# Kernel tuning notes

Hardware: AMD Instinct MI355X
Metric: run time of the kernel (lower is better)

Reference implementation:

```python
import jax, jax.numpy as jnp
import numpy as np

B, L = 4, 40960
C = 512
DMLP = 2048
TEMP = 1e-5
EPS = 1e-5
FACTOR = 2  # Smartpool factor at layer 4


def setup_inputs() -> dict:
    key = jax.random.key(0)
    ks = jax.random.split(key, 8)

    def w(k, shape, fan_in):
        return jax.random.normal(k, shape, jnp.float32) / np.float32(np.sqrt(fan_in))

    inp = {
        "x": jax.random.normal(ks[0], (B, 1, L), jnp.float32),
        "conv0_w": w(ks[1], (C, 1, 10), 10),   "conv0_b": jnp.zeros(C, jnp.float32),
        "conv1_w": w(ks[2], (C, C, 8), C * 8), "conv1_b": jnp.zeros(C, jnp.float32),
        "conv2_w": w(ks[3], (C, C, 4), C * 4), "conv2_b": jnp.zeros(C, jnp.float32),
        "conv3_w": w(ks[4], (C, C, 4), C * 4), "conv3_b": jnp.zeros(C, jnp.float32),
        "mlp_w1": w(ks[5], (C, DMLP), C),       "mlp_b1": jnp.zeros(DMLP, jnp.float32),
        "mlp_w2": w(ks[6], (DMLP, DMLP), DMLP), "mlp_b2": jnp.zeros(DMLP, jnp.float32),
        "mlp_w3": w(ks[7], (DMLP, 1), DMLP),    "mlp_b3": jnp.zeros(1, jnp.float32),
    }
    for i in range(5):  # ChannelNorm affine params (init: ones/zeros)
        inp[f"n{i}_w"] = jnp.ones(C, jnp.float32)
        inp[f"n{i}_b"] = jnp.zeros(C, jnp.float32)
    return inp


def _conv(x, w, b, stride, pad):
    # Conv1d with padding_mode='reflect': reflect-pad then VALID conv. x: [B,C,T]
    x = jnp.pad(x, ((0, 0), (0, 0), (pad, pad)), mode="reflect")
    y = jax.lax.conv_general_dilated(x, w, (stride,), "VALID",
                                     dimension_numbers=("NCH", "OIH", "NCH"))
    return y + b[None, :, None]


def _cnorm(x, g, b):
    # ChannelNorm: normalize over channel dim with unbiased variance (torch.var default)
    m = jnp.mean(x, axis=1, keepdims=True)
    v = jnp.var(x, axis=1, keepdims=True, ddof=1)
    return (x - m) * jax.lax.rsqrt(v + EPS) * g[None, :, None] + b[None, :, None]


def _forward(x, conv0_w, conv0_b, conv1_w, conv1_b, conv2_w, conv2_b, conv3_w, conv3_b,
             n0_w, n0_b, n1_w, n1_b, n2_w, n2_b, n3_w, n3_b, n4_w, n4_b,
             mlp_w1, mlp_b1, mlp_w2, mlp_b2, mlp_w3, mlp_b3):
    h = jax.nn.relu(_cnorm(_conv(x, conv0_w, conv0_b, 5, 3), n0_w, n0_b))
    h = jax.nn.relu(_cnorm(_conv(h, conv1_w, conv1_b, 4, 2), n1_w, n1_b))
    h = jax.nn.relu(_cnorm(_conv(h, conv2_w, conv2_b, 2, 1), n2_w, n2_b))
    h = jax.nn.relu(_cnorm(_conv(h, conv3_w, conv3_b, 2, 1), n3_w, n3_b))

    f = jnp.transpose(h, (0, 2, 1))  # [B,T,C]
    T = f.shape[1]

    # importance MLP (dropout inactive in eval), exact GELU, sigmoid head
    z = jax.nn.gelu(f @ mlp_w1 + mlp_b1, approximate=False)
    z = jax.nn.gelu(z @ mlp_w2 + mlp_b2, approximate=False)
    imp = jax.nn.sigmoid((z @ mlp_w3 + mlp_b3)[..., 0]) + TEMP          # [B,T]
    imp = imp / jnp.sum(imp, axis=1, keepdims=True) * (T / FACTOR)      # sums to T/factor

    # warp: cumsum -> ramp contributions -> 2x2 [[-1,1],[1,-1]] conv = double diff
    Tn = T // FACTOR  # == round(importance_cs[0,-1])
    cs = jnp.cumsum(imp, axis=1)                                        # [B,T]
    p = jnp.maximum(cs[:, :, None] - jnp.arange(Tn, dtype=cs.dtype)[None, None, :], 0.0)  # [B,T,Tn]
    pc = jnp.pad(p, ((0, 0), (0, 0), (0, 1)))
    d = pc[:, :, :-1] - pc[:, :, 1:]                                    # diff along new-time axis
    wmat = d - jnp.pad(d, ((0, 0), (1, 0), (0, 0)))[:, :-1, :]          # diff along old-time axis, [B,T,Tn]
    pooled = jnp.einsum("btn,btc->bnc", wmat, f)                        # interp_weights @ X

    out = jnp.transpose(pooled, (0, 2, 1))                              # [B,C,Tn]
    return jax.nn.relu(_cnorm(out, n4_w, n4_b))


def reference(x, conv0_w, conv0_b, conv1_w, conv1_b, conv2_w, conv2_b, conv3_w, conv3_b,
              n0_w, n0_b, n1_w, n1_b, n2_w, n2_b, n3_w, n3_b, n4_w, n4_b,
              mlp_w1, mlp_b1, mlp_w2, mlp_b2, mlp_w3, mlp_b3):
    return _forward(x, conv0_w, conv0_b, conv1_w, conv1_b, conv2_w, conv2_b, conv3_w, conv3_b,
                    n0_w, n0_b, n1_w, n1_b, n2_w, n2_b, n3_w, n3_b, n4_w, n4_b,
                    mlp_w1, mlp_b1, mlp_w2, mlp_b2, mlp_w3, mlp_b3)
```

## Files before the change

kernel.cpp:

```cpp
#include <hip/hip_runtime.h>
#include <hip/hip_bf16.h>
#include <math.h>

#define NB 4
#define LIN 40960
#define NC 512
#define T0 8192
#define T1 2048
#define T2 1024
#define T3 512
#define TN 256
#define DM 2048
#define EPSF 1e-5f
#define TEMPF 1e-5f

typedef __attribute__((ext_vector_type(8))) short bf16x8;
typedef __attribute__((ext_vector_type(4))) float f32x4;

__device__ __forceinline__ int refl(int t, int T) {
  if (t < 0) t = -t;
  if (t >= T) t = 2 * T - 2 - t;
  return t;
}

__device__ __forceinline__ void gld16(void* lds, const void* g) {
  __builtin_amdgcn_global_load_lds((const __attribute__((address_space(1))) unsigned int*)g,
                                   (__attribute__((address_space(3))) unsigned int*)lds, 16, 0, 0);
}

__device__ __forceinline__ void blk_sum2_512(float& a, float& b, float* scratch) {
#pragma unroll
  for (int off = 32; off > 0; off >>= 1) {
    a += __shfl_down(a, off, 64);
    b += __shfl_down(b, off, 64);
  }
  int lane = threadIdx.x & 63, wid = threadIdx.x >> 6;
  __syncthreads();
  if (lane == 0) { scratch[wid] = a; scratch[8 + wid] = b; }
  __syncthreads();
  float sa = 0.f, sb = 0.f;
#pragma unroll
  for (int i = 0; i < 8; i++) { sa += scratch[i]; sb += scratch[8 + i]; }
  a = sa; b = sb;
}

__device__ __forceinline__ void add_bf8(const __hip_bfloat16* p, float* v) {
  union { uint4 u; __hip_bfloat16 h[8]; } pk;
  pk.u = *(const uint4*)p;
#pragma unroll
  for (int j = 0; j < 8; j++) v[j] += __bfloat162float(pk.h[j]);
}

template <int KT>
__device__ __forceinline__ void prep_conv_body(const float* __restrict__ w, __hip_bfloat16* __restrict__ wt,
                                               int co, float* l) {
  const float* wb = w + (size_t)co * 512 * KT;
  for (int i = threadIdx.x; i < 512 * KT; i += 512) l[i] = wb[i];
  __syncthreads();
  __hip_bfloat16* wo = wt + (size_t)co * 512 * KT;
  for (int i = threadIdx.x; i < 512 * KT; i += 512) {
    int kk = i >> 9, ci = i & 511;
    wo[i] = __float2bfloat16(l[ci * KT + kk]);
  }
}

template <int KD, int ND>
__device__ __forceinline__ void prep_mlp_body(const float* __restrict__ w, __hip_bfloat16* __restrict__ wt,
                                              int bidx, float* sbuf) {
  float(*tile)[33] = (float(*)[33])sbuf;
  int bx = bidx % (ND / 32);
  int by = bidx / (ND / 32);
  int tx = threadIdx.x & 31, ty = threadIdx.x >> 5;
#pragma unroll
  for (int i = 0; i < 32; i += 16)
    tile[ty + i][tx] = w[(size_t)(by * 32 + ty + i) * ND + bx * 32 + tx];
  __syncthreads();
#pragma unroll
  for (int i = 0; i < 32; i += 16)
    wt[(size_t)(bx * 32 + ty + i) * KD + by * 32 + tx] = __float2bfloat16(tile[tx][ty + i]);
}

__device__ __forceinline__ void conv0_body(const float* __restrict__ x, const float* __restrict__ w,
                                           const float* __restrict__ bias, const float* __restrict__ gw,
                                           const float* __restrict__ gb, __hip_bfloat16* __restrict__ out,
                                           int blk, float* smem) {
  float* xv = smem;
  float* tb = smem + 64;
  float* stats = smem + 4672;
  int b = blk / (T0 / 8);
  int t0 = (blk % (T0 / 8)) * 8;
  int tid = threadIdx.x;
  if (tid < 45) xv[tid] = x[(size_t)b * LIN + refl(t0 * 5 - 3 + tid, LIN)];
  __syncthreads();
  float wk[10];
#pragma unroll
  for (int k = 0; k < 10; k++) wk[k] = w[tid * 10 + k];
  float bs = bias[tid];
  float acc[8];
#pragma unroll
  for (int tt = 0; tt < 8; tt++) {
    float a = bs;
#pragma unroll
    for (int k = 0; k < 10; k++) a += xv[tt * 5 + k] * wk[k];
    acc[tt] = a;
    tb[tid * 9 + tt] = a;
  }
  __syncthreads();
  int wave = tid >> 6, lane = tid & 63;
  float s = 0.f, q = 0.f;
#pragma unroll
  for (int j = 0; j < 8; j++) {
    float v = tb[(lane * 8 + j) * 9 + wave];
    s += v; q += v * v;
  }
#pragma unroll
  for (int off = 32; off > 0; off >>= 1) {
    s += __shfl_xor(s, off, 64);
    q += __shfl_xor(q, off, 64);
  }
  if (lane == 0) {
    float mean = s * (1.f / NC);
    float var = fmaxf((q - s * s * (1.f / NC)) * (1.f / (NC - 1)), 0.f);
    stats[wave] = mean;
    stats[8 + wave] = rsqrtf(var + EPSF);
  }
  __syncthreads();
  float gwv = gw[tid], gbv = gb[tid];
#pragma unroll
  for (int tt = 0; tt < 8; tt++) {
    float y = (acc[tt] - stats[tt]) * stats[8 + tt] * gwv + gbv;
    out[((size_t)(b * T0 + t0 + tt)) * NC + tid] = __float2bfloat16(fmaxf(y, 0.f));
  }
}

__global__ __launch_bounds__(512) void k_init(const float* x, const float* c0w, const float* c0b,
                                              const float* n0w, const float* n0b, __hip_bfloat16* h0b,
                                              const float* c1w, const float* c2w, const float* c3w,
                                              const float* mw1, const float* mw2,
                                              __hip_bfloat16* wt1, __hip_bfloat16* wt2,
                                              __hip_bfloat16* wt3, __hip_bfloat16* wm1t,
                                              __hip_bfloat16* wm2t) {
  __shared__ float smem[4688];
  int b = blockIdx.x;
  if (b < 4096) conv0_body(x, c0w, c0b, n0w, n0b, h0b, b, smem);
  else if (b < 4608) prep_conv_body<8>(c1w, wt1, b - 4096, smem);
  else if (b < 5120) prep_conv_body<4>(c2w, wt2, b - 4608, smem);
  else if (b < 5632) prep_conv_body<4>(c3w, wt3, b - 5120, smem);
  else if (b < 6656) prep_mlp_body<512, 2048>(mw1, wm1t, b - 5632, smem);
  else prep_mlp_body<2048, 2048>(mw2, wm2t, b - 6656, smem);
}

template <int MODE, int TIN_, int TOUT_, int SS, int PP, int KK, int NN, int SPLITK, int MM>
__global__ __launch_bounds__(256) void k_gemmB(const __hip_bfloat16* __restrict__ A,
                                               const __hip_bfloat16* __restrict__ Bt,
                                               __hip_bfloat16* __restrict__ Cp) {
  __shared__ __align__(16) __hip_bfloat16 sA[2][128 * 32];
  __shared__ __align__(16) __hip_bfloat16 sB[2][2][128 * 32];
  const int tid = threadIdx.x;
  const int lane = tid & 63;
  const int wave = tid >> 6;
  const int wm = wave >> 1, wn = wave & 1;
  constexpr int nt = NN / 128;
  constexpr int PS = (MM / 1024) * nt;
  constexpr int KBT = KK / 32;
  const int blk = blockIdx.x;
  const int xs = blk & 7, sl = blk >> 3;
  const int sk = sl / PS, rem = sl % PS;
  const int row0 = ((rem / nt) * 8 + xs) * 128;
  const int col0 = (rem % nt) * 128;
  const int kb0 = (sk * KBT) / SPLITK, kb1 = ((sk + 1) * KBT) / SPLITK;
  const int cq = lane >> 4, cl = lane & 15;

  const char* aP[2];
  const char* bP[2];

  auto stageA = [&](int kb, int buf) {
    bool recalc = (kb == kb0) || (MODE == 1 && (kb & 15) == 0);
    if (recalc) {
#pragma unroll
      for (int rr = 0; rr < 2; rr++) {
        int c = rr * 256 + tid;
        int m = c >> 2, kc = c & 3;
        int kcs = kc ^ (m & 3);
        size_t ga;
        if (MODE == 0) {
          ga = (size_t)(row0 + m) * KK + kb * 32 + kcs * 8;
        } else {
          int r = row0 + m;
          int bb = r / TOUT_;
          int t = r - bb * TOUT_;
          int k = (kb * 32) >> 9;
          int ci = ((kb * 32) & 511) + kcs * 8;
          int gt = refl(t * SS - PP + k, TIN_);
          ga = (((size_t)(bb * TIN_ + gt)) << 9) + ci;
        }
        aP[rr] = (const char*)(A + ga);
      }
    }
#pragma unroll
    for (int rr = 0; rr < 2; rr++) {
      gld16((char*)&sA[buf][0] + (rr * 256 + tid) * 16, aP[rr]);
      aP[rr] += 64;
    }
  };

  auto stageB = [&](int buf, bool doSub1) {
#pragma unroll
    for (int rr = 0; rr < 2; rr++) {
      gld16((char*)&sB[buf][0][0] + (rr * 256 + tid) * 16, bP[rr]);
      if (doSub1) gld16((char*)&sB[buf][1][0] + (rr * 256 + tid) * 16, bP[rr] + 64);
      bP[rr] += 128;
    }
  };

#pragma unroll
  for (int rr = 0; rr < 2; rr++) {
    int c = rr * 256 + tid;
    int n = c >> 2, kc = c & 3;
    int kcs = kc ^ (n & 3);
    bP[rr] = (const char*)(Bt + (size_t)(col0 + n) * KK + kb0 * 32 + kcs * 8);
  }

  f32x4 acc[4][4];
  const f32x4 zz = {0.f, 0.f, 0.f, 0.f};
#pragma unroll
  for (int mi = 0; mi < 4; mi++)
#pragma unroll
    for (int ni = 0; ni < 4; ni++) acc[mi][ni] = zz;

  stageA(kb0, 0);
  stageB(0, kb0 + 1 < kb1);

  const int p = cq ^ (cl & 3);
  for (int kb = kb0; kb < kb1; kb++) {
    const int jj = kb - kb0;
    __syncthreads();
    if (kb + 1 < kb1) stageA(kb + 1, (jj + 1) & 1);
    if (((jj & 1) == 0) && (kb + 2 < kb1)) stageB(((jj >> 1) + 1) & 1, kb + 3 < kb1);
    const short* bA = (const short*)&sA[jj & 1][0];
    const short* bB = (const short*)&sB[(jj >> 1) & 1][jj & 1][0];
    bf16x8 af[4], bfr[4];
#pragma unroll
    for (int mi = 0; mi < 4; mi++)
      af[mi] = *(const bf16x8*)(bA + (wm * 64 + mi * 16 + cl) * 32 + p * 8);
#pragma unroll
    for (int ni = 0; ni < 4; ni++)
      bfr[ni] = *(const bf16x8*)(bB + (wn * 64 + ni * 16 + cl) * 32 + p * 8);
#pragma unroll
    for (int mi = 0; mi < 4; mi++)
#pragma unroll
      for (int ni = 0; ni < 4; ni++)
        acc[mi][ni] = __builtin_amdgcn_mfma_f32_16x16x32_bf16(af[mi], bfr[ni], acc[mi][ni], 0, 0, 0);
  }

#pragma unroll
  for (int mi = 0; mi < 4; mi++)
#pragma unroll
    for (int ni = 0; ni < 4; ni++)
#pragma unroll
      for (int r2 = 0; r2 < 4; r2++) {
        int row = row0 + wm * 64 + mi * 16 + cq * 4 + r2;
        int col = col0 + wn * 64 + ni * 16 + cl;
        Cp[(size_t)sk * MM * NN + (size_t)row * NN + col] = __float2bfloat16(acc[mi][ni][r2]);
      }
}

template <int MODE, int TIN_, int TOUT_, int SS, int PP, int KK, int NN, int EPI, int SPLITK, int MM>
__global__ __launch_bounds__(256, 4) void k_gemmC(const __hip_bfloat16* __restrict__ A,
                                                  const __hip_bfloat16* __restrict__ Bt,
                                                  const float* __restrict__ bias,
                                                  __hip_bfloat16* __restrict__ Cout) {
  __shared__ __align__(16) __hip_bfloat16 sA[2][64 * 32];
  __shared__ __align__(16) __hip_bfloat16 sB[2][2][128 * 32];
  const int tid = threadIdx.x;
  const int lane = tid & 63;
  const int wave = tid >> 6;
  const int wm = wave >> 1, wn = wave & 1;
  constexpr int nt = NN / 128;
  constexpr int PS = (MM / 512) * nt;
  constexpr int KBT = KK / 32;
  const int blk = blockIdx.x;
  const int xs = blk & 7, sl = blk >> 3;
  const int sk = sl / PS, rem = sl % PS;
  const int row0 = ((rem / nt) * 8 + xs) * 64;
  const int col0 = (rem % nt) * 128;
  const int kb0 = (sk * KBT) / SPLITK, kb1 = ((sk + 1) * KBT) / SPLITK;
  const int cq = lane >> 4, cl = lane & 15;

  const char* aP;
  const char* bP[2];

  auto stageA = [&](int kb, int buf) {
    bool recalc = (kb == kb0) || (MODE == 1 && (kb & 15) == 0);
    if (recalc) {
      int m = tid >> 2, kc = tid & 3;
      int kcs = kc ^ (m & 3);
      size_t ga;
      if (MODE == 0) {
        ga = (size_t)(row0 + m) * KK + kb * 32 + kcs * 8;
      } else {
        int r = row0 + m;
        int bb = r / TOUT_;
        int t = r - bb * TOUT_;
        int k = (kb * 32) >> 9;
        int ci = ((kb * 32) & 511) + kcs * 8;
        int gt = refl(t * SS - PP + k, TIN_);
        ga = (((size_t)(bb * TIN_ + gt)) << 9) + ci;
      }
      aP = (const char*)(A + ga);
    }
    gld16((char*)&sA[buf][0] + tid * 16, aP);
    aP += 64;
  };

  auto stageB = [&](int buf, bool doSub1) {
#pragma unroll
    for (int rr = 0; rr < 2; rr++) {
      gld16((char*)&sB[buf][0][0] + (rr * 256 + tid) * 16, bP[rr]);
      if (doSub1) gld16((char*)&sB[buf][1][0] + (rr * 256 + tid) * 16, bP[rr] + 64);
      bP[rr] += 128;
    }
  };

#pragma unroll
  for (int rr = 0; rr < 2; rr++) {
    int c = rr * 256 + tid;
    int n = c >> 2, kc = c & 3;
    int kcs = kc ^ (n & 3);
    bP[rr] = (const char*)(Bt + (size_t)(col0 + n) * KK + kb0 * 32 + kcs * 8);
  }

  f32x4 acc[2][4];
  const f32x4 zz = {0.f, 0.f, 0.f, 0.f};
#pragma unroll
  for (int mi = 0; mi < 2; mi++)
#pragma unroll
    for (int ni = 0; ni < 4; ni++) acc[mi][ni] = zz;

  stageA(kb0, 0);
  stageB(0, kb0 + 1 < kb1);

  const int p = cq ^ (cl & 3);
  for (int kb = kb0; kb < kb1; kb++) {
    const int jj = kb - kb0;
    __syncthreads();
    if (kb + 1 < kb1) stageA(kb + 1, (jj + 1) & 1);
    if (((jj & 1) == 0) && (kb + 2 < kb1)) stageB(((jj >> 1) + 1) & 1, kb + 3 < kb1);
    const short* bA = (const short*)&sA[jj & 1][0];
    const short* bB = (const short*)&sB[(jj >> 1) & 1][jj & 1][0];
    bf16x8 af[2], bfr[4];
#pragma unroll
    for (int mi = 0; mi < 2; mi++)
      af[mi] = *(const bf16x8*)(bA + (wm * 32 + mi * 16 + cl) * 32 + p * 8);
#pragma unroll
    for (int ni = 0; ni < 4; ni++)
      bfr[ni] = *(const bf16x8*)(bB + (wn * 64 + ni * 16 + cl) * 32 + p * 8);
#pragma unroll
    for (int mi = 0; mi < 2; mi++)
#pragma unroll
      for (int ni = 0; ni < 4; ni++)
        acc[mi][ni] = __builtin_amdgcn_mfma_f32_16x16x32_bf16(af[mi], bfr[ni], acc[mi][ni], 0, 0, 0);
  }

#pragma unroll
  for (int mi = 0; mi < 2; mi++)
#pragma unroll
    for (int ni = 0; ni < 4; ni++)
#pragma unroll
      for (int r2 = 0; r2 < 4; r2++) {
        int row = row0 + wm * 32 + mi * 16 + cq * 4 + r2;
        int col = col0 + wn * 64 + ni * 16 + cl;
        float v = acc[mi][ni][r2];
        if (EPI == 1) {
          v += bias[col];
          v = 0.5f * v * (1.f + erff(v * 0.70710678118654752f));
          Cout[(size_t)row * NN + col] = __float2bfloat16(v);
        } else {
          Cout[(size_t)sk * MM * NN + (size_t)row * NN + col] = __float2bfloat16(v);
        }
      }
}

template <int NS>
__global__ __launch_bounds__(512) void k_cnorm(const __hip_bfloat16* __restrict__ g,
                                               const float* __restrict__ cb,
                                               const float* __restrict__ gw, const float* __restrict__ gb,
                                               __hip_bfloat16* __restrict__ out, size_t stride) {
  int wave = threadIdx.x >> 6, lane = threadIdx.x & 63;
  size_t row = (size_t)blockIdx.x * 8 + wave;
  float v[8];
  {
    float4 c0 = *(const float4*)(cb + lane * 8), c1 = *(const float4*)(cb + lane * 8 + 4);
    v[0] = c0.x; v[1] = c0.y; v[2] = c0.z; v[3] = c0.w;
    v[4] = c1.x; v[5] = c1.y; v[6] = c1.z; v[7] = c1.w;
  }
#pragma unroll
  for (int s = 0; s < NS; s++) add_bf8(g + s * stride + row * NC + lane * 8, v);
  float s = 0.f, q = 0.f;
#pragma unroll
  for (int j = 0; j < 8; j++) { s += v[j]; q += v[j] * v[j]; }
#pragma unroll
  for (int off = 32; off > 0; off >>= 1) {
    s += __shfl_xor(s, off, 64);
    q += __shfl_xor(q, off, 64);
  }
  float mean = s * (1.f / NC);
  float var = fmaxf((q - s * s * (1.f / NC)) * (1.f / (NC - 1)), 0.f);
  float rstd = rsqrtf(var + EPSF);
  float4 w0 = *(const float4*)(gw + lane * 8), w1 = *(const float4*)(gw + lane * 8 + 4);
  float4 b0 = *(const float4*)(gb + lane * 8), b1 = *(const float4*)(gb + lane * 8 + 4);
  float gwv[8] = {w0.x, w0.y, w0.z, w0.w, w1.x, w1.y, w1.z, w1.w};
  float gbv[8] = {b0.x, b0.y, b0.z, b0.w, b1.x, b1.y, b1.z, b1.w};
  union { __hip_bfloat16 h[8]; uint4 u; } pk;
#pragma unroll
  for (int j = 0; j < 8; j++)
    pk.h[j] = __float2bfloat16(fmaxf((v[j] - mean) * rstd * gwv[j] + gbv[j], 0.f));
  *(uint4*)(out + row * NC + lane * 8) = pk.u;
}

template <int NS>
__global__ __launch_bounds__(256) void k_head(const __hip_bfloat16* __restrict__ g,
                                              const float* __restrict__ b2,
                                              const float* __restrict__ w3, const float* __restrict__ b3,
                                              float* __restrict__ imp) {
  __shared__ float red[4];
  int row = blockIdx.x, tid = threadIdx.x;
  int c = tid * 8;
  float v[8];
  {
    float4 x0 = *(const float4*)(b2 + c), x1 = *(const float4*)(b2 + c + 4);
    v[0] = x0.x; v[1] = x0.y; v[2] = x0.z; v[3] = x0.w;
    v[4] = x1.x; v[5] = x1.y; v[6] = x1.z; v[7] = x1.w;
  }
#pragma unroll
  for (int s = 0; s < NS; s++) add_bf8(g + (size_t)s * (2048 * DM) + (size_t)row * DM + c, v);
  float a = 0.f;
  float4 w0 = *(const float4*)(w3 + c), w1 = *(const float4*)(w3 + c + 4);
  float wv[8] = {w0.x, w0.y, w0.z, w0.w, w1.x, w1.y, w1.z, w1.w};
#pragma unroll
  for (int j = 0; j < 8; j++) {
    float z = 0.5f * v[j] * (1.f + erff(v[j] * 0.70710678118654752f));
    a += z * wv[j];
  }
#pragma unroll
  for (int off = 32; off > 0; off >>= 1) a += __shfl_down(a, off, 64);
  int lane = tid & 63, wid = tid >> 6;
  if (lane == 0) red[wid] = a;
  __syncthreads();
  if (tid == 0) {
    float s = red[0] + red[1] + red[2] + red[3] + b3[0];
    imp[row] = 1.f / (1.f + expf(-s)) + TEMPF;
  }
}

__device__ __forceinline__ float dfun(float cv, int n) {
  float d = fmaxf(cv - (float)n, 0.f);
  if (n < TN - 1) d = fminf(d, 1.f);
  return d;
}

__global__ __launch_bounds__(512) void k_poolfinal(const __hip_bfloat16* __restrict__ f,
                                                   const float* __restrict__ imp,
                                                   const float* __restrict__ gw, const float* __restrict__ gb,
                                                   float* __restrict__ out) {
  __shared__ float wt[T3];
  __shared__ float wsum[8];
  __shared__ float red[16];
  int b = blockIdx.x / TN, n = blockIdx.x % TN;
  int tid = threadIdx.x, wave = tid >> 6, lane = tid & 63;
  float own = imp[b * T3 + tid];
  float s = own;
#pragma unroll
  for (int off = 1; off < 64; off <<= 1) {
    float t = __shfl_up(s, off, 64);
    if (lane >= off) s += t;
  }
  if (lane == 63) wsum[wave] = s;
  __syncthreads();
  float prefix = 0.f, total = 0.f;
#pragma unroll
  for (int w = 0; w < 8; w++) {
    float ws_ = wsum[w];
    total += ws_;
    if (w < wave) prefix += ws_;
  }
  float scale = (float)TN / total;
  float incl = (prefix + s) * scale;
  float excl = (prefix + s - own) * scale;
  wt[tid] = dfun(incl, n) - dfun(excl, n);
  __syncthreads();
  float acc = 0.f;
  for (int t = 0; t < T3; t++) {
    float w = wt[t];
    if (w != 0.f) acc += w * __bfloat162float(f[((size_t)b * T3 + t) * NC + tid]);
  }
  float sv = acc, q = acc * acc;
  blk_sum2_512(sv, q, red);
  float mean = sv * (1.f / NC);
  float var = fmaxf((q - sv * sv * (1.f / NC)) * (1.f / (NC - 1)), 0.f);
  float y = (acc - mean) * rsqrtf(var + EPSF) * gw[tid] + gb[tid];
  out[((size_t)b * NC + tid) * TN + n] = fmaxf(y, 0.f);
}

extern "C" void kernel_launch(void* const* d_in, const int* in_sizes, int n_in,
                              void* d_out, int out_size, void* d_ws, size_t ws_size,
                              hipStream_t stream) {
  const float* x   = (const float*)d_in[0];
  const float* c0w = (const float*)d_in[1];  const float* c0b = (const float*)d_in[2];
  const float* c1w = (const float*)d_in[3];  const float* c1b = (const float*)d_in[4];
  const float* c2w = (const float*)d_in[5];  const float* c2b = (const float*)d_in[6];
  const float* c3w = (const float*)d_in[7];  const float* c3b = (const float*)d_in[8];
  const float* mw1 = (const float*)d_in[9];  const float* mb1 = (const float*)d_in[10];
  const float* mw2 = (const float*)d_in[11]; const float* mb2 = (const float*)d_in[12];
  const float* mw3 = (const float*)d_in[13]; const float* mb3 = (const float*)d_in[14];
  const float* n0w = (const float*)d_in[15]; const float* n0b = (const float*)d_in[16];
  const float* n1w = (const float*)d_in[17]; const float* n1b = (const float*)d_in[18];
  const float* n2w = (const float*)d_in[19]; const float* n2b = (const float*)d_in[20];
  const float* n3w = (const float*)d_in[21]; const float* n3b = (const float*)d_in[22];
  const float* n4w = (const float*)d_in[23]; const float* n4b = (const float*)d_in[24];

  char* base = (char*)d_ws;
  __hip_bfloat16* h0b  = (__hip_bfloat16*)(base);
  __hip_bfloat16* h1b  = (__hip_bfloat16*)(base);
  __hip_bfloat16* h2b  = (__hip_bfloat16*)(base + (8u << 20));
  __hip_bfloat16* h3b  = (__hip_bfloat16*)(base + (12u << 20));
  __hip_bfloat16* z1b  = (__hip_bfloat16*)(base + (14u << 20));
  float*          imp  = (float*)(base + (22u << 20));
  __hip_bfloat16* g    = (__hip_bfloat16*)(base + (32u << 20));
  __hip_bfloat16* wm1t = (__hip_bfloat16*)(base + (64u << 20));
  __hip_bfloat16* wt2  = (__hip_bfloat16*)(base + (66u << 20));
  __hip_bfloat16* wt3  = (__hip_bfloat16*)(base + (68u << 20));
  __hip_bfloat16* wt1  = (__hip_bfloat16*)(base + (70u << 20));
  __hip_bfloat16* wm2t = (__hip_bfloat16*)(base + (74u << 20));
  float* outp = (float*)d_out;

  k_init<<<4096 + 6656, 512, 0, stream>>>(x, c0w, c0b, n0w, n0b, h0b,
                                          c1w, c2w, c3w, mw1, mw2, wt1, wt2, wt3, wm1t, wm2t);

  k_gemmB<1, 8192, 2048, 4, 2, 4096, 512, 3, 8192><<<768, 256, 0, stream>>>(h0b, wt1, g);
  k_cnorm<3><<<8192 / 8, 512, 0, stream>>>(g, c1b, n1w, n1b, h1b, (size_t)8192 * 512);
  k_gemmB<1, 2048, 1024, 2, 1, 2048, 512, 6, 4096><<<768, 256, 0, stream>>>(h1b, wt2, g);
  k_cnorm<6><<<4096 / 8, 512, 0, stream>>>(g, c2b, n2w, n2b, h2b, (size_t)4096 * 512);
  k_gemmC<1, 1024, 512, 2, 1, 2048, 512, 0, 6, 2048><<<768, 256, 0, stream>>>(h2b, wt3, c3b, g);
  k_cnorm<6><<<2048 / 8, 512, 0, stream>>>(g, c3b, n3w, n3b, h3b, (size_t)2048 * 512);
  k_gemmC<0, 0, 1, 0, 0, 512, 2048, 1, 1, 2048><<<512, 256, 0, stream>>>(h3b, wm1t, mb1, z1b);
  k_gemmB<0, 0, 1, 0, 0, 2048, 2048, 3, 2048><<<768, 256, 0, stream>>>(z1b, wm2t, g);

  k_head<3><<<NB * T3, 256, 0, stream>>>(g, mb2, mw3, mb3, imp);
  k_poolfinal<<<NB * TN, 512, 0, stream>>>(h3b, imp, n4w, n4b, outp);
}
```

Measured before the change: 315.1 us.

## Switch GEMM kernels to triple-buffered LDS pipeline with explicit vmcnt waits

Both bf16 MFMA GEMM kernels used double buffering of A, with B loaded two k-steps at a time, and a full __syncthreads each step. They now use a three-slot ring for A and B, prefetching two k-steps ahead. Each step waits with a partial s_waitcnt vmcnt so only the oldest stage must have landed, then issues a raw s_barrier. This keeps more global loads in flight and drops the full drain at every barrier, but LDS use goes up and correctness depends on the hand-set vmcnt counts matching the number of loads issued per stage.

```diff
diff --git a/kernel.cpp b/kernel.cpp
--- a/kernel.cpp
+++ b/kernel.cpp
@@ -154,8 +154,8 @@
 __global__ __launch_bounds__(256) void k_gemmB(const __hip_bfloat16* __restrict__ A,
                                                const __hip_bfloat16* __restrict__ Bt,
                                                __hip_bfloat16* __restrict__ Cp) {
-  __shared__ __align__(16) __hip_bfloat16 sA[2][128 * 32];
-  __shared__ __align__(16) __hip_bfloat16 sB[2][2][128 * 32];
+  __shared__ __align__(16) __hip_bfloat16 sA[3][128 * 32];
+  __shared__ __align__(16) __hip_bfloat16 sB[3][128 * 32];
   const int tid = threadIdx.x;
   const int lane = tid & 63;
   const int wave = tid >> 6;
@@ -204,12 +204,11 @@
     }
   };
 
-  auto stageB = [&](int buf, bool doSub1) {
+  auto stageB = [&](int buf) {
 #pragma unroll
     for (int rr = 0; rr < 2; rr++) {
-      gld16((char*)&sB[buf][0][0] + (rr * 256 + tid) * 16, bP[rr]);
-      if (doSub1) gld16((char*)&sB[buf][1][0] + (rr * 256 + tid) * 16, bP[rr] + 64);
-      bP[rr] += 128;
+      gld16((char*)&sB[buf][0] + (rr * 256 + tid) * 16, bP[rr]);
+      bP[rr] += 64;
     }
   };
 
@@ -228,17 +227,20 @@
 #pragma unroll
     for (int ni = 0; ni < 4; ni++) acc[mi][ni] = zz;
 
+  const int NS = kb1 - kb0;
   stageA(kb0, 0);
-  stageB(0, kb0 + 1 < kb1);
+  stageB(0);
+  if (NS > 1) { stageA(kb0 + 1, 1); stageB(1); }
 
   const int p = cq ^ (cl & 3);
-  for (int kb = kb0; kb < kb1; kb++) {
-    const int jj = kb - kb0;
-    __syncthreads();
-    if (kb + 1 < kb1) stageA(kb + 1, (jj + 1) & 1);
-    if (((jj & 1) == 0) && (kb + 2 < kb1)) stageB(((jj >> 1) + 1) & 1, kb + 3 < kb1);
-    const short* bA = (const short*)&sA[jj & 1][0];
-    const short* bB = (const short*)&sB[(jj >> 1) & 1][jj & 1][0];
+  int slot = 0, slot2 = 2;
+  for (int jj = 0; jj < NS; ++jj) {
+    if (jj + 1 < NS) { asm volatile("s_waitcnt vmcnt(4)" ::: "memory"); }
+    else             { asm volatile("s_waitcnt vmcnt(0)" ::: "memory"); }
+    __builtin_amdgcn_s_barrier();
+    if (jj + 2 < NS) { stageA(kb0 + jj + 2, slot2); stageB(slot2); }
+    const short* bA = (const short*)&sA[slot][0];
+    const short* bB = (const short*)&sB[slot][0];
     bf16x8 af[4], bfr[4];
 #pragma unroll
     for (int mi = 0; mi < 4; mi++)
@@ -251,6 +253,8 @@
 #pragma unroll
       for (int ni = 0; ni < 4; ni++)
         acc[mi][ni] = __builtin_amdgcn_mfma_f32_16x16x32_bf16(af[mi], bfr[ni], acc[mi][ni], 0, 0, 0);
+    slot = (slot == 2) ? 0 : slot + 1;
+    slot2 = (slot2 == 2) ? 0 : slot2 + 1;
   }
 
 #pragma unroll
@@ -270,8 +274,8 @@
                                                   const __hip_bfloat16* __restrict__ Bt,
                                                   const float* __restrict__ bias,
                                                   __hip_bfloat16* __restrict__ Cout) {
-  __shared__ __align__(16) __hip_bfloat16 sA[2][64 * 32];
-  __shared__ __align__(16) __hip_bfloat16 sB[2][2][128 * 32];
+  __shared__ __align__(16) __hip_bfloat16 sA[3][64 * 32];
+  __shared__ __align__(16) __hip_bfloat16 sB[3][128 * 32];
   const int tid = threadIdx.x;
   const int lane = tid & 63;
   const int wave = tid >> 6;
@@ -313,12 +317,11 @@
     aP += 64;
   };
 
-  auto stageB = [&](int buf, bool doSub1) {
+  auto stageB = [&](int buf) {
 #pragma unroll
     for (int rr = 0; rr < 2; rr++) {
-      gld16((char*)&sB[buf][0][0] + (rr * 256 + tid) * 16, bP[rr]);
-      if (doSub1) gld16((char*)&sB[buf][1][0] + (rr * 256 + tid) * 16, bP[rr] + 64);
-      bP[rr] += 128;
+      gld16((char*)&sB[buf][0] + (rr * 256 + tid) * 16, bP[rr]);
+      bP[rr] += 64;
     }
   };
 
@@ -337,17 +340,20 @@
 #pragma unroll
     for (int ni = 0; ni < 4; ni++) acc[mi][ni] = zz;
 
+  const int NS = kb1 - kb0;
   stageA(kb0, 0);
-  stageB(0, kb0 + 1 < kb1);
+  stageB(0);
+  if (NS > 1) { stageA(kb0 + 1, 1); stageB(1); }
 
   const int p = cq ^ (cl & 3);
-  for (int kb = kb0; kb < kb1; kb++) {
-    const int jj = kb - kb0;
-    __syncthreads();
-    if (kb + 1 < kb1) stageA(kb + 1, (jj + 1) & 1);
-    if (((jj & 1) == 0) && (kb + 2 < kb1)) stageB(((jj >> 1) + 1) & 1, kb + 3 < kb1);
-    const short* bA = (const short*)&sA[jj & 1][0];
-    const short* bB = (const short*)&sB[(jj >> 1) & 1][jj & 1][0];
+  int slot = 0, slot2 = 2;
+  for (int jj = 0; jj < NS; ++jj) {
+    if (jj + 1 < NS) { asm volatile("s_waitcnt vmcnt(3)" ::: "memory"); }
+    else             { asm volatile("s_waitcnt vmcnt(0)" ::: "memory"); }
+    __builtin_amdgcn_s_barrier();
+    if (jj + 2 < NS) { stageA(kb0 + jj + 2, slot2); stageB(slot2); }
+    const short* bA = (const short*)&sA[slot][0];
+    const short* bB = (const short*)&sB[slot][0];
     bf16x8 af[2], bfr[4];
 #pragma unroll
     for (int mi = 0; mi < 2; mi++)
@@ -360,6 +366,8 @@
 #pragma unroll
       for (int ni = 0; ni < 4; ni++)
         acc[mi][ni] = __builtin_amdgcn_mfma_f32_16x16x32_bf16(af[mi], bfr[ni], acc[mi][ni], 0, 0, 0);
+    slot = (slot == 2) ? 0 : slot + 1;
+    slot2 = (slot2 == 2) ? 0 : slot2 + 1;
   }
 
 #pragma unroll
```

Result: no change. 320.3 us (+1.7%).

## Add 256x256-tile split-K GEMM kernel for conv1 and MLP layer 2

Applied to the files above, without the earlier changes.

Adds a new GEMM kernel using 256x256 output tiles, 512 threads (8 waves), and double-buffered LDS stages that each hold two 32-wide K slices. Global loads for the next stage are interleaved across the four compute sub-steps, and the kernel raises wave priority around the MFMA block. It replaces the 128-tile kernel for conv1 and the second MLP layer, with split-K raised from 3 to 4 and the downstream reductions updated to match. Larger tiles cut redundant global/LDS traffic per FLOP, but the grid shrinks to 256 blocks. The kernel also needs more registers and LDS, which could hurt occupancy.

```diff
diff --git a/kernel.cpp b/kernel.cpp
--- a/kernel.cpp
+++ b/kernel.cpp
@@ -148,6 +148,152 @@
   else if (b < 5632) prep_conv_body<4>(c3w, wt3, b - 5120, smem);
   else if (b < 6656) prep_mlp_body<512, 2048>(mw1, wm1t, b - 5632, smem);
   else prep_mlp_body<2048, 2048>(mw2, wm2t, b - 6656, smem);
+}
+
+template <int MODE, int TIN_, int TOUT_, int SS, int PP, int KK, int NN, int SPLITK, int MM>
+__global__ __launch_bounds__(512, 2) void k_gemmE(const __hip_bfloat16* __restrict__ A,
+                                                  const __hip_bfloat16* __restrict__ Bt,
+                                                  __hip_bfloat16* __restrict__ Cp) {
+  __shared__ __align__(16) __hip_bfloat16 sA[2][2][256 * 32];
+  __shared__ __align__(16) __hip_bfloat16 sB[2][2][256 * 32];
+  const int tid = threadIdx.x;
+  const int lane = tid & 63;
+  const int wave = tid >> 6;
+  const int wm = wave >> 2, wn = wave & 3;
+  constexpr int nt = NN / 256;
+  constexpr int PS = (MM / 2048) * nt;
+  constexpr int KBT = KK / 32;
+  constexpr int NT = KBT / (2 * SPLITK);
+  const int blk = blockIdx.x;
+  const int xs = blk & 7, sl = blk >> 3;
+  const int sk = sl / PS, rem = sl % PS;
+  const int row0 = ((rem / nt) * 8 + xs) * 256;
+  const int col0 = (rem % nt) * 256;
+  const int kb0 = sk * (KBT / SPLITK);
+  const int cq = lane >> 4, cl = lane & 15;
+
+  const char* aP[2];
+  const char* bP[2];
+
+  auto stageA = [&](int kb, int buf, int kk) {
+    bool recalc = (kb == kb0) || (MODE == 1 && (kb & 15) == 0);
+    if (recalc) {
+#pragma unroll
+      for (int rr = 0; rr < 2; rr++) {
+        int c = rr * 512 + tid;
+        int m = c >> 2, kc = c & 3;
+        int kcs = kc ^ (m & 3);
+        size_t ga;
+        if (MODE == 0) {
+          ga = (size_t)(row0 + m) * KK + kb * 32 + kcs * 8;
+        } else {
+          int r = row0 + m;
+          int bb = r / TOUT_;
+          int t = r - bb * TOUT_;
+          int k = (kb * 32) >> 9;
+          int ci = ((kb * 32) & 511) + kcs * 8;
+          int gt = refl(t * SS - PP + k, TIN_);
+          ga = (((size_t)(bb * TIN_ + gt)) << 9) + ci;
+        }
+        aP[rr] = (const char*)(A + ga);
+      }
+    }
+#pragma unroll
+    for (int rr = 0; rr < 2; rr++) {
+      gld16((char*)&sA[buf][kk][0] + (rr * 512 + tid) * 16, aP[rr]);
+      aP[rr] += 64;
+    }
+  };
+
+  auto stageB = [&](int buf, int kk) {
+#pragma unroll
+    for (int rr = 0; rr < 2; rr++) {
+      gld16((char*)&sB[buf][kk][0] + (rr * 512 + tid) * 16, bP[rr]);
+      bP[rr] += 64;
+    }
+  };
+
+#pragma unroll
+  for (int rr = 0; rr < 2; rr++) {
+    int c = rr * 512 + tid;
+    int n = c >> 2, kc = c & 3;
+    int kcs = kc ^ (n & 3);
+    bP[rr] = (const char*)(Bt + (size_t)(col0 + n) * KK + kb0 * 32 + kcs * 8);
+  }
+
+  f32x4 acc[8][4];
+  const f32x4 zz = {0.f, 0.f, 0.f, 0.f};
+#pragma unroll
+  for (int mi = 0; mi < 8; mi++)
+#pragma unroll
+    for (int ni = 0; ni < 4; ni++) acc[mi][ni] = zz;
+
+  stageA(kb0, 0, 0);
+  stageB(0, 0);
+  stageA(kb0 + 1, 0, 1);
+  stageB(0, 1);
+  asm volatile("s_waitcnt vmcnt(0)" ::: "memory");
+  __builtin_amdgcn_s_barrier();
+
+  const int p = cq ^ (cl & 3);
+  for (int t = 0; t < NT; ++t) {
+    const int buf = t & 1;
+    const int kbase = kb0 + 2 * t;
+    const short* bA0 = (const short*)&sA[buf][0][0];
+    const short* bA1 = (const short*)&sA[buf][1][0];
+    const short* bB0 = (const short*)&sB[buf][0][0];
+    const short* bB1 = (const short*)&sB[buf][1][0];
+    bf16x8 bfr0[4], bfr1[4];
+#pragma unroll
+    for (int q = 0; q < 4; ++q) {
+      bf16x8 af0[2], af1[2];
+      if (q == 0) {
+#pragma unroll
+        for (int ni = 0; ni < 4; ni++) {
+          bfr0[ni] = *(const bf16x8*)(bB0 + (wn * 64 + ni * 16 + cl) * 32 + p * 8);
+          bfr1[ni] = *(const bf16x8*)(bB1 + (wn * 64 + ni * 16 + cl) * 32 + p * 8);
+        }
+      }
+#pragma unroll
+      for (int i = 0; i < 2; i++) {
+        int mi = q * 2 + i;
+        af0[i] = *(const bf16x8*)(bA0 + (wm * 128 + mi * 16 + cl) * 32 + p * 8);
+        af1[i] = *(const bf16x8*)(bA1 + (wm * 128 + mi * 16 + cl) * 32 + p * 8);
+      }
+      if (t + 1 < NT) {
+        if (q == 0) stageA(kbase + 2, buf ^ 1, 0);
+        else if (q == 1) stageB(buf ^ 1, 0);
+        else if (q == 2) stageA(kbase + 3, buf ^ 1, 1);
+        else stageB(buf ^ 1, 1);
+      }
+      __builtin_amdgcn_s_barrier();
+      asm volatile("s_waitcnt lgkmcnt(0)" ::: "memory");
+      __builtin_amdgcn_s_setprio(1);
+#pragma unroll
+      for (int i = 0; i < 2; i++)
+#pragma unroll
+        for (int ni = 0; ni < 4; ni++) {
+          acc[q * 2 + i][ni] =
+              __builtin_amdgcn_mfma_f32_16x16x32_bf16(af0[i], bfr0[ni], acc[q * 2 + i][ni], 0, 0, 0);
+          acc[q * 2 + i][ni] =
+              __builtin_amdgcn_mfma_f32_16x16x32_bf16(af1[i], bfr1[ni], acc[q * 2 + i][ni], 0, 0, 0);
+        }
+      __builtin_amdgcn_s_setprio(0);
+      if (q == 3 && t + 1 < NT) asm volatile("s_waitcnt vmcnt(0)" ::: "memory");
+      __builtin_amdgcn_s_barrier();
+    }
+  }
+
+#pragma unroll
+  for (int mi = 0; mi < 8; mi++)
+#pragma unroll
+    for (int ni = 0; ni < 4; ni++)
+#pragma unroll
+      for (int r2 = 0; r2 < 4; r2++) {
+        int row = row0 + wm * 128 + mi * 16 + cq * 4 + r2;
+        int col = col0 + wn * 64 + ni * 16 + cl;
+        Cp[(size_t)sk * MM * NN + (size_t)row * NN + col] = __float2bfloat16(acc[mi][ni][r2]);
+      }
 }
 
 template <int MODE, int TIN_, int TOUT_, int SS, int PP, int KK, int NN, int SPLITK, int MM>
@@ -537,15 +683,15 @@
   k_init<<<4096 + 6656, 512, 0, stream>>>(x, c0w, c0b, n0w, n0b, h0b,
                                           c1w, c2w, c3w, mw1, mw2, wt1, wt2, wt3, wm1t, wm2t);
 
-  k_gemmB<1, 8192, 2048, 4, 2, 4096, 512, 3, 8192><<<768, 256, 0, stream>>>(h0b, wt1, g);
-  k_cnorm<3><<<8192 / 8, 512, 0, stream>>>(g, c1b, n1w, n1b, h1b, (size_t)8192 * 512);
+  k_gemmE<1, 8192, 2048, 4, 2, 4096, 512, 4, 8192><<<256, 512, 0, stream>>>(h0b, wt1, g);
+  k_cnorm<4><<<8192 / 8, 512, 0, stream>>>(g, c1b, n1w, n1b, h1b, (size_t)8192 * 512);
   k_gemmB<1, 2048, 1024, 2, 1, 2048, 512, 6, 4096><<<768, 256, 0, stream>>>(h1b, wt2, g);
   k_cnorm<6><<<4096 / 8, 512, 0, stream>>>(g, c2b, n2w, n2b, h2b, (size_t)4096 * 512);
   k_gemmC<1, 1024, 512, 2, 1, 2048, 512, 0, 6, 2048><<<768, 256, 0, stream>>>(h2b, wt3, c3b, g);
   k_cnorm<6><<<2048 / 8, 512, 0, stream>>>(g, c3b, n3w, n3b, h3b, (size_t)2048 * 512);
   k_gemmC<0, 0, 1, 0, 0, 512, 2048, 1, 1, 2048><<<512, 256, 0, stream>>>(h3b, wm1t, mb1, z1b);
-  k_gemmB<0, 0, 1, 0, 0, 2048, 2048, 3, 2048><<<768, 256, 0, stream>>>(z1b, wm2t, g);
-
-  k_head<3><<<NB * T3, 256, 0, stream>>>(g, mb2, mw3, mb3, imp);
+  k_gemmE<0, 0, 1, 0, 0, 2048, 2048, 4, 2048><<<256, 512, 0, stream>>>(z1b, wm2t, g);
+
+  k_head<4><<<NB * T3, 256, 0, stream>>>(g, mb2, mw3, mb3, imp);
   k_poolfinal<<<NB * TN, 512, 0, stream>>>(h3b, imp, n4w, n4b, outp);
 }
```

Result: slower. 326.5 us (+3.6%).

## Fuse MLP head and smart-pool kernels into one cooperative launch with grid sync

Applied to the files above, without the earlier changes.

Merges the importance head and the pooling/final norm kernels into a single cooperative kernel of 256 blocks. Each block first computes 8 importance rows, then all blocks wait on a grid-wide sync and each block handles 4 pooled output positions. This removes one kernel launch and the gap between launches. In exchange each kernel has far fewer blocks, per-row work runs serially inside a block, and the grid barrier adds its own cost.

```diff
diff --git a/kernel.cpp b/kernel.cpp
--- a/kernel.cpp
+++ b/kernel.cpp
@@ -1,5 +1,6 @@
 #include <hip/hip_runtime.h>
 #include <hip/hip_bf16.h>
+#include <hip/hip_cooperative_groups.h>
 #include <math.h>
 
 #define NB 4
@@ -418,88 +419,102 @@
   *(uint4*)(out + row * NC + lane * 8) = pk.u;
 }
 
-template <int NS>
-__global__ __launch_bounds__(256) void k_head(const __hip_bfloat16* __restrict__ g,
-                                              const float* __restrict__ b2,
-                                              const float* __restrict__ w3, const float* __restrict__ b3,
-                                              float* __restrict__ imp) {
-  __shared__ float red[4];
-  int row = blockIdx.x, tid = threadIdx.x;
-  int c = tid * 8;
-  float v[8];
-  {
-    float4 x0 = *(const float4*)(b2 + c), x1 = *(const float4*)(b2 + c + 4);
-    v[0] = x0.x; v[1] = x0.y; v[2] = x0.z; v[3] = x0.w;
-    v[4] = x1.x; v[5] = x1.y; v[6] = x1.z; v[7] = x1.w;
-  }
-#pragma unroll
-  for (int s = 0; s < NS; s++) add_bf8(g + (size_t)s * (2048 * DM) + (size_t)row * DM + c, v);
-  float a = 0.f;
-  float4 w0 = *(const float4*)(w3 + c), w1 = *(const float4*)(w3 + c + 4);
-  float wv[8] = {w0.x, w0.y, w0.z, w0.w, w1.x, w1.y, w1.z, w1.w};
-#pragma unroll
-  for (int j = 0; j < 8; j++) {
-    float z = 0.5f * v[j] * (1.f + erff(v[j] * 0.70710678118654752f));
-    a += z * wv[j];
-  }
-#pragma unroll
-  for (int off = 32; off > 0; off >>= 1) a += __shfl_down(a, off, 64);
-  int lane = tid & 63, wid = tid >> 6;
-  if (lane == 0) red[wid] = a;
-  __syncthreads();
-  if (tid == 0) {
-    float s = red[0] + red[1] + red[2] + red[3] + b3[0];
-    imp[row] = 1.f / (1.f + expf(-s)) + TEMPF;
-  }
-}
-
 __device__ __forceinline__ float dfun(float cv, int n) {
   float d = fmaxf(cv - (float)n, 0.f);
   if (n < TN - 1) d = fminf(d, 1.f);
   return d;
 }
 
-__global__ __launch_bounds__(512) void k_poolfinal(const __hip_bfloat16* __restrict__ f,
-                                                   const float* __restrict__ imp,
-                                                   const float* __restrict__ gw, const float* __restrict__ gb,
-                                                   float* __restrict__ out) {
+__global__ __launch_bounds__(512) void k_tail(const __hip_bfloat16* __restrict__ g,
+                                              const float* __restrict__ b2,
+                                              const float* __restrict__ w3, const float* __restrict__ b3,
+                                              float* __restrict__ imp,
+                                              const __hip_bfloat16* __restrict__ f,
+                                              const float* __restrict__ gw, const float* __restrict__ gb,
+                                              float* __restrict__ out) {
+  __shared__ float red[16];
   __shared__ float wt[T3];
   __shared__ float wsum[8];
-  __shared__ float red[16];
-  int b = blockIdx.x / TN, n = blockIdx.x % TN;
-  int tid = threadIdx.x, wave = tid >> 6, lane = tid & 63;
-  float own = imp[b * T3 + tid];
-  float s = own;
-#pragma unroll
-  for (int off = 1; off < 64; off <<= 1) {
-    float t = __shfl_up(s, off, 64);
-    if (lane >= off) s += t;
-  }
-  if (lane == 63) wsum[wave] = s;
-  __syncthreads();
-  float prefix = 0.f, total = 0.f;
-#pragma unroll
-  for (int w = 0; w < 8; w++) {
-    float ws_ = wsum[w];
-    total += ws_;
-    if (w < wave) prefix += ws_;
-  }
-  float scale = (float)TN / total;
-  float incl = (prefix + s) * scale;
-  float excl = (prefix + s - own) * scale;
-  wt[tid] = dfun(incl, n) - dfun(excl, n);
-  __syncthreads();
-  float acc = 0.f;
-  for (int t = 0; t < T3; t++) {
-    float w = wt[t];
-    if (w != 0.f) acc += w * __bfloat162float(f[((size_t)b * T3 + t) * NC + tid]);
-  }
-  float sv = acc, q = acc * acc;
-  blk_sum2_512(sv, q, red);
-  float mean = sv * (1.f / NC);
-  float var = fmaxf((q - sv * sv * (1.f / NC)) * (1.f / (NC - 1)), 0.f);
-  float y = (acc - mean) * rsqrtf(var + EPSF) * gw[tid] + gb[tid];
-  out[((size_t)b * NC + tid) * TN + n] = fmaxf(y, 0.f);
+  const int tid = threadIdx.x, lane = tid & 63, wid = tid >> 6;
+
+#pragma unroll 1
+  for (int rr = 0; rr < 8; rr++) {
+    int row = blockIdx.x * 8 + rr;
+    int c = tid * 4;
+    float v[4];
+    {
+      float4 x0 = *(const float4*)(b2 + c);
+      v[0] = x0.x; v[1] = x0.y; v[2] = x0.z; v[3] = x0.w;
+    }
+#pragma unroll
+    for (int s = 0; s < 3; s++) {
+      union { uint2 u; __hip_bfloat16 h[4]; } pk;
+      pk.u = *(const uint2*)(g + (size_t)s * (2048 * DM) + (size_t)row * DM + c);
+#pragma unroll
+      for (int j = 0; j < 4; j++) v[j] += __bfloat162float(pk.h[j]);
+    }
+    float4 w0 = *(const float4*)(w3 + c);
+    float wv[4] = {w0.x, w0.y, w0.z, w0.w};
+    float a = 0.f;
+#pragma unroll
+    for (int j = 0; j < 4; j++) {
+      float z = 0.5f * v[j] * (1.f + erff(v[j] * 0.70710678118654752f));
+      a += z * wv[j];
+    }
+#pragma unroll
+    for (int off = 32; off > 0; off >>= 1) a += __shfl_down(a, off, 64);
+    __syncthreads();
+    if (lane == 0) red[wid] = a;
+    __syncthreads();
+    if (tid == 0) {
+      float s = b3[0];
+#pragma unroll
+      for (int i = 0; i < 8; i++) s += red[i];
+      imp[row] = 1.f / (1.f + expf(-s)) + TEMPF;
+    }
+  }
+
+  cooperative_groups::this_grid().sync();
+
+#pragma unroll 1
+  for (int q = 0; q < 4; q++) {
+    __syncthreads();
+    int idx = blockIdx.x * 4 + q;
+    int b = idx / TN, n = idx % TN;
+    int wave = wid;
+    float own = imp[b * T3 + tid];
+    float s = own;
+#pragma unroll
+    for (int off = 1; off < 64; off <<= 1) {
+      float t = __shfl_up(s, off, 64);
+      if (lane >= off) s += t;
+    }
+    if (lane == 63) wsum[wave] = s;
+    __syncthreads();
+    float prefix = 0.f, total = 0.f;
+#pragma unroll
+    for (int w = 0; w < 8; w++) {
+      float ws_ = wsum[w];
+      total += ws_;
+      if (w < wave) prefix += ws_;
+    }
+    float scale = (float)TN / total;
+    float incl = (prefix + s) * scale;
+    float excl = (prefix + s - own) * scale;
+    wt[tid] = dfun(incl, n) - dfun(excl, n);
+    __syncthreads();
+    float acc = 0.f;
+    for (int t = 0; t < T3; t++) {
+      float w = wt[t];
+      if (w != 0.f) acc += w * __bfloat162float(f[((size_t)b * T3 + t) * NC + tid]);
+    }
+    float sv = acc, qq = acc * acc;
+    blk_sum2_512(sv, qq, red);
+    float mean = sv * (1.f / NC);
+    float var = fmaxf((qq - sv * sv * (1.f / NC)) * (1.f / (NC - 1)), 0.f);
+    float y = (acc - mean) * rsqrtf(var + EPSF) * gw[tid] + gb[tid];
+    out[((size_t)b * NC + tid) * TN + n] = fmaxf(y, 0.f);
+  }
 }
 
 extern "C" void kernel_launch(void* const* d_in, const int* in_sizes, int n_in,
@@ -546,6 +561,17 @@
   k_gemmC<0, 0, 1, 0, 0, 512, 2048, 1, 1, 2048><<<512, 256, 0, stream>>>(h3b, wm1t, mb1, z1b);
   k_gemmB<0, 0, 1, 0, 0, 2048, 2048, 3, 2048><<<768, 256, 0, stream>>>(z1b, wm2t, g);
 
-  k_head<3><<<NB * T3, 256, 0, stream>>>(g, mb2, mw3, mb3, imp);
-  k_poolfinal<<<NB * TN, 512, 0, stream>>>(h3b, imp, n4w, n4b, outp);
-}
+  {
+    const __hip_bfloat16* g_c = g;
+    const float* b2_c = mb2;
+    const float* w3_c = mw3;
+    const float* b3_c = mb3;
+    float* imp_c = imp;
+    const __hip_bfloat16* f_c = h3b;
+    const float* gw_c = n4w;
+    const float* gb_c = n4b;
+    float* out_c = outp;
+    void* args[9] = {&g_c, &b2_c, &w3_c, &b3_c, &imp_c, &f_c, &gw_c, &gb_c, &out_c};
+    hipLaunchCooperativeKernel((const void*)k_tail, dim3(256), dim3(512), args, 0, stream);
+  }
+}
```

Result: slower. 459.7 us (+45.9%).
